# Optimization experiments

Hardware: AMD Instinct MI355X
Metric: run time of the kernel (lower is better)

## Reference

```python
import jax, jax.numpy as jnp
import numpy as np

B, C, H, W = 4, 256, 64, 64
INTER = C // 2
BN_EPS = 1e-5


def setup_inputs() -> dict:
    key = jax.random.key(0)
    ks = jax.random.split(key, 12)
    s = 0.05
    return {
        "x": jax.random.normal(ks[0], (B, C, H, W), dtype=jnp.float32),
        "theta_w": jax.random.normal(ks[1], (INTER, C), dtype=jnp.float32) * s,
        "theta_b": jax.random.normal(ks[2], (INTER,), dtype=jnp.float32) * s,
        "phi_w": jax.random.normal(ks[3], (INTER, C), dtype=jnp.float32) * s,
        "phi_b": jax.random.normal(ks[4], (INTER,), dtype=jnp.float32) * s,
        "g_w": jax.random.normal(ks[5], (INTER, C), dtype=jnp.float32) * s,
        "g_b": jax.random.normal(ks[6], (INTER,), dtype=jnp.float32) * s,
        "W_w": jax.random.normal(ks[7], (C, INTER), dtype=jnp.float32) * s,
        "W_b": jax.random.normal(ks[8], (C,), dtype=jnp.float32) * s,
        "bn_gamma": jnp.ones((C,), dtype=jnp.float32),
        "bn_beta": jnp.zeros((C,), dtype=jnp.float32),
    }


def _conv1x1(x, w, b):
    # 1x1 conv == per-pixel GEMM: (B,C,H,W) x (O,C) -> (B,O,H,W)
    return jnp.einsum("bchw,oc->bohw", x, w) + b[None, :, None, None]


def reference(x, theta_w, theta_b, phi_w, phi_b, g_w, g_b, W_w, W_b, bn_gamma, bn_beta):
    b, c, h, w = x.shape
    hw = h * w
    theta = _conv1x1(x, theta_w, theta_b).reshape(b, -1, hw)  # (B, inter, HW) -> queries
    phi = _conv1x1(x, phi_w, phi_b).reshape(b, -1, hw)        # (B, inter, HW) -> keys
    g = _conv1x1(x, g_w, g_b).reshape(b, -1, hw)              # (B, inter, HW) -> values
    # f[n,m] = <theta[:,n], phi[:,m]> over all HW spatial positions
    f = jnp.einsum("bin,bim->bnm", theta, phi)                # (B, HW, HW)
    attn = jax.nn.softmax(f, axis=-1)
    y = jnp.einsum("bnm,bim->bin", attn, g)                   # (B, inter, HW)
    y = y.reshape(b, c // 2, h, w)
    wy = _conv1x1(y, W_w, W_b)                                # (B, C, H, W)
    # BatchNorm2d (training-mode batch statistics, per channel)
    mean = jnp.mean(wy, axis=(0, 2, 3), keepdims=True)
    var = jnp.var(wy, axis=(0, 2, 3), keepdims=True)
    wy_bn = bn_gamma[None, :, None, None] * (wy - mean) * jax.lax.rsqrt(var + BN_EPS) + bn_beta[None, :, None, None]
    return wy_bn + x
```

## Files before the change

### kernel.cpp

```cpp
#include <hip/hip_runtime.h>
#include <hip/hip_bf16.h>

#define HWN   4096
#define CIN   256
#define NINTER 128
#define NBATCH 4
#define BN_EPS 1e-5f
#define NC    4
#define CHUNK 1024
#define LOG2E 1.4426950408889634f
#define SMAX  64.0f

typedef __bf16 bf16_t;
typedef __bf16 bf16x8 __attribute__((ext_vector_type(8)));
typedef __bf16 bf16x4 __attribute__((ext_vector_type(4)));
typedef float  f32x4  __attribute__((ext_vector_type(4)));
typedef float  f32x16 __attribute__((ext_vector_type(16)));

__device__ __forceinline__ float fexp2(float x) {
  return __builtin_amdgcn_exp2f(x);
}

__device__ __forceinline__ void split_bf16(float v, bf16_t& h, bf16_t& l) {
  h = (bf16_t)v;
  l = (bf16_t)(v - (float)h);
}

#define OFF_QH  0
#define OFF_KH  4194304
#define OFF_V   8388608
#define OFF_OP  12582912
#define OFF_WY  46137344
#define OFF_LP  54525952
#define OFF_WBF 54790144
#define OFF_ST  55314432

__global__ __launch_bounds__(256) void convert_weights(
    const float* __restrict__ tw, const float* __restrict__ pw,
    const float* __restrict__ gw, const float* __restrict__ ww,
    bf16_t* __restrict__ out) {
  int i = blockIdx.x * 256 + threadIdx.x;
  float v;
  if (i < 32768)        v = tw[i];
  else if (i < 65536)   v = pw[i - 32768];
  else if (i < 98304)   v = gw[i - 65536];
  else                  v = ww[i - 98304];
  bf16_t h, l;
  split_bf16(v, h, l);
  out[i] = h;
  out[131072 + i] = l;
}

__global__ __launch_bounds__(256, 4) void qkv_kernel(
    const float* __restrict__ x, const bf16_t* __restrict__ wbf,
    const float* __restrict__ tb, const float* __restrict__ pb,
    const float* __restrict__ gb,
    bf16_t* __restrict__ Qh, bf16_t* __restrict__ Kh, bf16_t* __restrict__ V) {
  const int ntb  = blockIdx.x;
  const int b    = blockIdx.y;
  const int tid  = threadIdx.x;
  const int lane = tid & 63;
  const int wv   = tid >> 6;
  const int l31  = lane & 31;
  const int half = lane >> 5;

  __shared__ __align__(16) bf16_t smem[4608];
  bf16_t (*xTh)[72] = (bf16_t(*)[72])smem;
  bf16_t (*xTl)[72] = (bf16_t(*)[72])(smem + 2304);
  bf16_t (*Tr)[136] = (bf16_t(*)[136])smem;

  const bf16_t* Th = wbf;
  const bf16_t* Tl = wbf + 131072;
  const bf16_t* Ph = wbf + 32768;
  const bf16_t* Pl = wbf + 131072 + 32768;
  const bf16_t* Gh = wbf + 65536;
  const float*  xb = x + (size_t)b * CIN * HWN + ntb * 32;

  f32x16 aq, ak, av;
#pragma unroll
  for (int i = 0; i < 16; i++) { aq[i] = 0.f; ak[i] = 0.f; av[i] = 0.f; }

  for (int c0 = 0; c0 < 256; c0 += 64) {
    __syncthreads();
#pragma unroll
    for (int i = 0; i < 8; i++) {
      int idx = tid + i * 256;
      int cc = idx >> 5;
      int nn = idx & 31;
      float v = xb[(size_t)(c0 + cc) * HWN + nn];
      bf16_t h, l;
      split_bf16(v, h, l);
      xTh[nn][cc] = h;
      xTl[nn][cc] = l;
    }
    __syncthreads();
#pragma unroll
    for (int kk = 0; kk < 64; kk += 16) {
      size_t woff = (size_t)(32 * wv + l31) * 256 + c0 + kk + half * 8;
      bf16x8 th = *(const bf16x8*)(Th + woff);
      bf16x8 tl = *(const bf16x8*)(Tl + woff);
      bf16x8 ph = *(const bf16x8*)(Ph + woff);
      bf16x8 pl = *(const bf16x8*)(Pl + woff);
      bf16x8 gh = *(const bf16x8*)(Gh + woff);
      bf16x8 bh = *(const bf16x8*)(&xTh[l31][kk + half * 8]);
      bf16x8 bl = *(const bf16x8*)(&xTl[l31][kk + half * 8]);
      aq = __builtin_amdgcn_mfma_f32_32x32x16_bf16(th, bh, aq, 0, 0, 0);
      aq = __builtin_amdgcn_mfma_f32_32x32x16_bf16(th, bl, aq, 0, 0, 0);
      aq = __builtin_amdgcn_mfma_f32_32x32x16_bf16(tl, bh, aq, 0, 0, 0);
      ak = __builtin_amdgcn_mfma_f32_32x32x16_bf16(ph, bh, ak, 0, 0, 0);
      ak = __builtin_amdgcn_mfma_f32_32x32x16_bf16(ph, bl, ak, 0, 0, 0);
      ak = __builtin_amdgcn_mfma_f32_32x32x16_bf16(pl, bh, ak, 0, 0, 0);
      av = __builtin_amdgcn_mfma_f32_32x32x16_bf16(gh, bh, av, 0, 0, 0);
    }
  }

  const int trow = tid >> 3;
  const int tc16 = (tid & 7) * 16;
  bf16_t* qh = Qh + ((size_t)b * HWN + ntb * 32) * NINTER;
  bf16_t* kh = Kh + ((size_t)b * HWN + ntb * 32) * NINTER;

#pragma unroll
  for (int rnd = 0; rnd < 2; rnd++) {
    __syncthreads();
#pragma unroll
    for (int rg = 0; rg < 4; rg++) {
      int och0 = 32 * wv + 8 * rg + 4 * half;
#pragma unroll
      for (int j = 0; j < 4; j++) {
        float v = (rnd == 0) ? (aq[rg * 4 + j] + tb[och0 + j]) * LOG2E
                             : (ak[rg * 4 + j] + pb[och0 + j]);
        Tr[l31][och0 + j] = (bf16_t)v;
      }
    }
    __syncthreads();
    bf16_t* dst = (rnd == 0) ? qh : kh;
    bf16x8 v0 = *(const bf16x8*)(&Tr[trow][tc16]);
    bf16x8 v1 = *(const bf16x8*)(&Tr[trow][tc16 + 8]);
    *(bf16x8*)(dst + (size_t)trow * NINTER + tc16) = v0;
    *(bf16x8*)(dst + (size_t)trow * NINTER + tc16 + 8) = v1;
  }

  const int n = ntb * 32 + l31;
  bf16_t* vd = V + (size_t)b * NINTER * HWN;
#pragma unroll
  for (int r = 0; r < 16; r++) {
    int och = 32 * wv + (r & 3) + 8 * (r >> 2) + 4 * half;
    vd[(size_t)och * HWN + n] = (bf16_t)(av[r] + gb[och]);
  }
}

__global__ __launch_bounds__(256, 2) void attn_kernel(
    const bf16_t* __restrict__ Qh, const bf16_t* __restrict__ Kh,
    const bf16_t* __restrict__ V,
    float* __restrict__ Opart, float* __restrict__ Lp) {
  const int qt    = blockIdx.x;
  const int chunk = blockIdx.y;
  const int b     = blockIdx.z;
  const int tid   = threadIdx.x;
  const int lane  = tid & 63;
  const int wv    = tid >> 6;
  const int l15   = lane & 15;
  const int quad  = lane >> 4;
  const int kbase = chunk * CHUNK;

  __shared__ __align__(16) bf16_t Klds[32][136];
  __shared__ __align__(16) bf16_t Vlds[144][56];
  __shared__ __align__(16) bf16_t Plds[4][32][40];

  const bf16_t* Qhb = Qh + (size_t)b * HWN * NINTER;
  const bf16_t* Khb = Kh + (size_t)b * HWN * NINTER;
  const bf16_t* Vb  = V + (size_t)b * NINTER * HWN;

  if (tid < 112) {
    int row = 128 + tid / 7;
    int c8 = (tid % 7) * 8;
    bf16x8 v;
#pragma unroll
    for (int j = 0; j < 8; j++) v[j] = (bf16_t)((row == 128) ? 1.0f : 0.0f);
    *(bf16x8*)(&Vlds[row][c8]) = v;
  }

  bf16x8 qf[2][4];
#pragma unroll
  for (int qs = 0; qs < 2; qs++) {
    const int qrow = qt * 128 + wv * 32 + qs * 16 + l15;
#pragma unroll
    for (int kc = 0; kc < 4; kc++)
      qf[qs][kc] = *(const bf16x8*)(Qhb + (size_t)qrow * NINTER + kc * 32 + quad * 8);
  }

  f32x4 o[2][8], ol[2];
#pragma unroll
  for (int qs = 0; qs < 2; qs++) {
#pragma unroll
    for (int dt = 0; dt < 8; dt++)
#pragma unroll
      for (int i = 0; i < 4; i++) o[qs][dt][i] = 0.f;
#pragma unroll
    for (int i = 0; i < 4; i++) ol[qs][i] = 0.f;
  }

  for (int t = 0; t < 32; t++) {
    __syncthreads();
#pragma unroll
    for (int i = 0; i < 2; i++) {
      int idx = tid + i * 256;
      int row = idx >> 4;
      int c8 = (idx & 15) * 8;
      *(uint4*)(&Klds[row][c8]) =
          *(const uint4*)(Khb + (size_t)(kbase + t * 32 + row) * NINTER + c8);
    }
#pragma unroll
    for (int i = 0; i < 2; i++) {
      int idx = tid + i * 256;
      int row = idx >> 2;
      int c8 = (idx & 3) * 8;
      *(uint4*)(&Vlds[row][c8]) =
          *(const uint4*)(Vb + (size_t)row * HWN + kbase + t * 32 + c8);
    }
    __syncthreads();

    f32x4 s[2][2];
#pragma unroll
    for (int qs = 0; qs < 2; qs++)
#pragma unroll
      for (int ks = 0; ks < 2; ks++)
#pragma unroll
        for (int i = 0; i < 4; i++) s[qs][ks][i] = 0.f;
#pragma unroll
    for (int ks = 0; ks < 2; ks++)
#pragma unroll
      for (int kc = 0; kc < 4; kc++) {
        bf16x8 kf = *(const bf16x8*)(&Klds[ks * 16 + l15][kc * 32 + quad * 8]);
        s[0][ks] = __builtin_amdgcn_mfma_f32_16x16x32_bf16(kf, qf[0][kc], s[0][ks], 0, 0, 0);
        s[1][ks] = __builtin_amdgcn_mfma_f32_16x16x32_bf16(kf, qf[1][kc], s[1][ks], 0, 0, 0);
      }

#pragma unroll
    for (int qs = 0; qs < 2; qs++)
#pragma unroll
      for (int ks = 0; ks < 2; ks++) {
        bf16x4 p4;
#pragma unroll
        for (int r = 0; r < 4; r++)
          p4[r] = (bf16_t)fexp2(s[qs][ks][r] - SMAX);
        *(bf16x4*)(&Plds[wv][qs * 16 + l15][ks * 16 + quad * 4]) = p4;
      }

    bf16x8 pf0 = *(const bf16x8*)(&Plds[wv][l15][quad * 8]);
    bf16x8 pf1 = *(const bf16x8*)(&Plds[wv][16 + l15][quad * 8]);
#pragma unroll
    for (int dt = 0; dt < 8; dt++) {
      bf16x8 vf = *(const bf16x8*)(&Vlds[dt * 16 + l15][quad * 8]);
      o[0][dt] = __builtin_amdgcn_mfma_f32_16x16x32_bf16(pf0, vf, o[0][dt], 0, 0, 0);
      o[1][dt] = __builtin_amdgcn_mfma_f32_16x16x32_bf16(pf1, vf, o[1][dt], 0, 0, 0);
    }
    bf16x8 vfl = *(const bf16x8*)(&Vlds[128 + l15][quad * 8]);
    ol[0] = __builtin_amdgcn_mfma_f32_16x16x32_bf16(pf0, vfl, ol[0], 0, 0, 0);
    ol[1] = __builtin_amdgcn_mfma_f32_16x16x32_bf16(pf1, vfl, ol[1], 0, 0, 0);
  }

  float* Ob = Opart + ((size_t)(b * NC + chunk) * HWN) * NINTER;
#pragma unroll
  for (int qs = 0; qs < 2; qs++)
#pragma unroll
    for (int r = 0; r < 4; r++) {
      int n = qt * 128 + wv * 32 + qs * 16 + quad * 4 + r;
#pragma unroll
      for (int dt = 0; dt < 8; dt++)
        Ob[(size_t)n * NINTER + dt * 16 + l15] = o[qs][dt][r];
      if (l15 == 0)
        Lp[(size_t)(b * NC + chunk) * HWN + n] = ol[qs][r];
    }
}

__global__ __launch_bounds__(256, 4) void wconv_kernel(
    const bf16_t* __restrict__ Wbf, const float* __restrict__ Opart,
    const float* __restrict__ Lp, const float* __restrict__ Wb,
    bf16_t* __restrict__ WY) {
  const int ntb = blockIdx.x;
  const int b   = blockIdx.y;
  const int tid = threadIdx.x;
  const int lane = tid & 63;
  const int wv   = tid >> 6;
  const int l31  = lane & 31;
  const int half = lane >> 5;

  __shared__ __align__(16) bf16_t Ylds[32][136];
  __shared__ float Linv[32];

  if (tid < 32) {
    int n = ntb * 32 + tid;
    float ls = 0.f;
#pragma unroll
    for (int c = 0; c < NC; c++) ls += Lp[(size_t)(b * NC + c) * HWN + n];
    Linv[tid] = 1.f / ls;
  }

  const int nrow = tid >> 3;
  const int dgrp = tid & 7;
  float oacc[16];
#pragma unroll
  for (int j = 0; j < 16; j++) oacc[j] = 0.f;
#pragma unroll
  for (int c = 0; c < NC; c++) {
    const float* Op = Opart +
        ((size_t)(b * NC + c) * HWN + ntb * 32 + nrow) * NINTER + dgrp * 16;
#pragma unroll
    for (int q = 0; q < 4; q++) {
      f32x4 v = *(const f32x4*)(Op + q * 4);
#pragma unroll
      for (int j = 0; j < 4; j++) oacc[q * 4 + j] += v[j];
    }
  }
  __syncthreads();
  {
    float inv = Linv[nrow];
    bf16x8 y0, y1;
#pragma unroll
    for (int j = 0; j < 8; j++) {
      y0[j] = (bf16_t)(oacc[j] * inv);
      y1[j] = (bf16_t)(oacc[8 + j] * inv);
    }
    *(bf16x8*)(&Ylds[nrow][dgrp * 16]) = y0;
    *(bf16x8*)(&Ylds[nrow][dgrp * 16 + 8]) = y1;
  }
  __syncthreads();

  const bf16_t* Wh = Wbf + 98304;
  f32x16 acc[2];
#pragma unroll
  for (int c = 0; c < 2; c++)
#pragma unroll
    for (int i = 0; i < 16; i++) acc[c][i] = 0.f;

#pragma unroll
  for (int k0 = 0; k0 < 128; k0 += 16) {
    bf16x8 a0 = *(const bf16x8*)(Wh + (size_t)(wv * 64 + l31) * NINTER + k0 + half * 8);
    bf16x8 a1 = *(const bf16x8*)(Wh + (size_t)(wv * 64 + 32 + l31) * NINTER + k0 + half * 8);
    bf16x8 b0 = *(const bf16x8*)(&Ylds[l31][k0 + half * 8]);
    acc[0] = __builtin_amdgcn_mfma_f32_32x32x16_bf16(a0, b0, acc[0], 0, 0, 0);
    acc[1] = __builtin_amdgcn_mfma_f32_32x32x16_bf16(a1, b0, acc[1], 0, 0, 0);
  }

  bf16_t* dst = WY + (size_t)b * 256 * HWN + ntb * 32;
#pragma unroll
  for (int ct = 0; ct < 2; ct++)
#pragma unroll
    for (int r = 0; r < 16; r++) {
      int co = wv * 64 + ct * 32 + (r & 3) + 8 * (r >> 2) + 4 * half;
      dst[(size_t)co * HWN + l31] = (bf16_t)(acc[ct][r] + Wb[co]);
    }
}

__global__ __launch_bounds__(256) void stats_kernel(
    const bf16_t* __restrict__ WY, float* __restrict__ stats) {
  const int c = blockIdx.x;
  const int tid = threadIdx.x;
  float s = 0.f, s2 = 0.f;
  for (int b = 0; b < NBATCH; b++) {
    const bf16_t* p = WY + ((size_t)b * 256 + c) * HWN;
    for (int i = tid * 8; i < HWN; i += 2048) {
      bf16x8 v8 = *(const bf16x8*)(p + i);
#pragma unroll
      for (int j = 0; j < 8; j++) {
        float v = (float)v8[j];
        s += v;
        s2 += v * v;
      }
    }
  }
#pragma unroll
  for (int off = 1; off < 64; off <<= 1) {
    s += __shfl_xor(s, off);
    s2 += __shfl_xor(s2, off);
  }
  __shared__ float red[8];
  int wv = tid >> 6;
  if ((tid & 63) == 0) { red[wv] = s; red[4 + wv] = s2; }
  __syncthreads();
  if (tid == 0) {
    float S = red[0] + red[1] + red[2] + red[3];
    float S2 = red[4] + red[5] + red[6] + red[7];
    float mean = S * (1.f / 16384.f);
    float var = S2 * (1.f / 16384.f) - mean * mean;
    stats[c] = mean;
    stats[256 + c] = rsqrtf(var + BN_EPS);
  }
}

__global__ __launch_bounds__(256) void bn_kernel(
    const bf16_t* __restrict__ WY, const float* __restrict__ x,
    const float* __restrict__ stats, const float* __restrict__ gamma,
    const float* __restrict__ beta, float* __restrict__ out) {
  int idx = blockIdx.x * 256 + threadIdx.x;
  int e = idx * 4;
  int c = (e >> 12) & 255;
  bf16x4 w4 = *(const bf16x4*)(WY + e);
  float4 xv = *(const float4*)(x + e);
  float mean = stats[c];
  float g = gamma[c] * stats[256 + c];
  float bb = beta[c];
  float4 o;
  o.x = g * ((float)w4[0] - mean) + bb + xv.x;
  o.y = g * ((float)w4[1] - mean) + bb + xv.y;
  o.z = g * ((float)w4[2] - mean) + bb + xv.z;
  o.w = g * ((float)w4[3] - mean) + bb + xv.w;
  *(float4*)(out + e) = o;
}

extern "C" void kernel_launch(void* const* d_in, const int* in_sizes, int n_in,
                              void* d_out, int out_size, void* d_ws, size_t ws_size,
                              hipStream_t stream) {
  const float* x       = (const float*)d_in[0];
  const float* theta_b = (const float*)d_in[2];
  const float* phi_b   = (const float*)d_in[4];
  const float* g_b     = (const float*)d_in[6];
  const float* W_b     = (const float*)d_in[8];
  const float* bn_g    = (const float*)d_in[9];
  const float* bn_b    = (const float*)d_in[10];
  float* out = (float*)d_out;

  char* ws = (char*)d_ws;
  bf16_t* Qh  = (bf16_t*)(ws + OFF_QH);
  bf16_t* Kh  = (bf16_t*)(ws + OFF_KH);
  bf16_t* V   = (bf16_t*)(ws + OFF_V);
  float*  OP  = (float*)(ws + OFF_OP);
  bf16_t* WY  = (bf16_t*)(ws + OFF_WY);
  float*  LP  = (float*)(ws + OFF_LP);
  bf16_t* WBF = (bf16_t*)(ws + OFF_WBF);
  float*  ST  = (float*)(ws + OFF_ST);

  convert_weights<<<512, 256, 0, stream>>>(
      (const float*)d_in[1], (const float*)d_in[3],
      (const float*)d_in[5], (const float*)d_in[7], WBF);
  qkv_kernel<<<dim3(128, NBATCH), 256, 0, stream>>>(
      x, WBF, theta_b, phi_b, g_b, Qh, Kh, V);
  attn_kernel<<<dim3(32, NC, NBATCH), 256, 0, stream>>>(
      Qh, Kh, V, OP, LP);
  wconv_kernel<<<dim3(128, NBATCH), 256, 0, stream>>>(
      WBF, OP, LP, W_b, WY);
  stats_kernel<<<256, 256, 0, stream>>>(WY, ST);
  bn_kernel<<<4096, 256, 0, stream>>>(WY, x, ST, bn_g, bn_b, out);
}
```

Baseline: 180.8 us.

## Register-prefetch K/V tiles in attention and split keys into eight chunks

The attention loop now prefetches the next K/V tile into registers while the current tile is computed from LDS, ping-ponging between two register sets with explicit barriers and scheduling fences. The key split becomes a template parameter, and eight chunks are used when the workspace is large enough, which doubles the grid to give more parallelism. Launch bounds rise to three blocks per SM. The aim is to hide global load latency and raise occupancy, at the cost of more register pressure and twice the partial-output traffic and reduction work in wconv.

```diff
diff --git a/kernel.cpp b/kernel.cpp
--- a/kernel.cpp
+++ b/kernel.cpp
@@ -6,8 +6,6 @@
 #define NINTER 128
 #define NBATCH 4
 #define BN_EPS 1e-5f
-#define NC    4
-#define CHUNK 1024
 #define LOG2E 1.4426950408889634f
 #define SMAX  64.0f
 
@@ -25,15 +23,6 @@
   h = (bf16_t)v;
   l = (bf16_t)(v - (float)h);
 }
-
-#define OFF_QH  0
-#define OFF_KH  4194304
-#define OFF_V   8388608
-#define OFF_OP  12582912
-#define OFF_WY  46137344
-#define OFF_LP  54525952
-#define OFF_WBF 54790144
-#define OFF_ST  55314432
 
 __global__ __launch_bounds__(256) void convert_weights(
     const float* __restrict__ tw, const float* __restrict__ pw,
@@ -149,10 +138,13 @@
   }
 }
 
-__global__ __launch_bounds__(256, 2) void attn_kernel(
+template<int NCv>
+__global__ __launch_bounds__(256, 3) void attn_kernel(
     const bf16_t* __restrict__ Qh, const bf16_t* __restrict__ Kh,
     const bf16_t* __restrict__ V,
     float* __restrict__ Opart, float* __restrict__ Lp) {
+  constexpr int CH = HWN / NCv;
+  constexpr int NT = CH / 32;
   const int qt    = blockIdx.x;
   const int chunk = blockIdx.y;
   const int b     = blockIdx.z;
@@ -161,7 +153,7 @@
   const int wv    = tid >> 6;
   const int l15   = lane & 15;
   const int quad  = lane >> 4;
-  const int kbase = chunk * CHUNK;
+  const int kbase = chunk * CH;
 
   __shared__ __align__(16) bf16_t Klds[32][136];
   __shared__ __align__(16) bf16_t Vlds[144][56];
@@ -200,26 +192,32 @@
     for (int i = 0; i < 4; i++) ol[qs][i] = 0.f;
   }
 
-  for (int t = 0; t < 32; t++) {
-    __syncthreads();
+  auto load_tile = [&](uint4* kr, uint4* vr, int t) {
 #pragma unroll
     for (int i = 0; i < 2; i++) {
       int idx = tid + i * 256;
-      int row = idx >> 4;
-      int c8 = (idx & 15) * 8;
-      *(uint4*)(&Klds[row][c8]) =
-          *(const uint4*)(Khb + (size_t)(kbase + t * 32 + row) * NINTER + c8);
+      kr[i] = *(const uint4*)(Khb + (size_t)(kbase + t * 32 + (idx >> 4)) * NINTER + (idx & 15) * 8);
     }
 #pragma unroll
     for (int i = 0; i < 2; i++) {
       int idx = tid + i * 256;
-      int row = idx >> 2;
-      int c8 = (idx & 3) * 8;
-      *(uint4*)(&Vlds[row][c8]) =
-          *(const uint4*)(Vb + (size_t)row * HWN + kbase + t * 32 + c8);
-    }
-    __syncthreads();
-
+      vr[i] = *(const uint4*)(Vb + (size_t)(idx >> 2) * HWN + kbase + t * 32 + (idx & 3) * 8);
+    }
+  };
+  auto store_tile = [&](const uint4* kr, const uint4* vr) {
+#pragma unroll
+    for (int i = 0; i < 2; i++) {
+      int idx = tid + i * 256;
+      *(uint4*)(&Klds[idx >> 4][(idx & 15) * 8]) = kr[i];
+    }
+#pragma unroll
+    for (int i = 0; i < 2; i++) {
+      int idx = tid + i * 256;
+      *(uint4*)(&Vlds[idx >> 2][(idx & 3) * 8]) = vr[i];
+    }
+  };
+
+  auto compute = [&]() {
     f32x4 s[2][2];
 #pragma unroll
     for (int qs = 0; qs < 2; qs++)
@@ -258,9 +256,39 @@
     bf16x8 vfl = *(const bf16x8*)(&Vlds[128 + l15][quad * 8]);
     ol[0] = __builtin_amdgcn_mfma_f32_16x16x32_bf16(pf0, vfl, ol[0], 0, 0, 0);
     ol[1] = __builtin_amdgcn_mfma_f32_16x16x32_bf16(pf1, vfl, ol[1], 0, 0, 0);
-  }
-
-  float* Ob = Opart + ((size_t)(b * NC + chunk) * HWN) * NINTER;
+  };
+
+  uint4 krA[2], vrA[2], krB[2], vrB[2];
+  load_tile(krA, vrA, 0);
+
+#pragma unroll 1
+  for (int t = 0; t < NT; t += 2) {
+    __builtin_amdgcn_s_barrier();
+    __builtin_amdgcn_sched_barrier(0);
+    store_tile(krA, vrA);
+    __builtin_amdgcn_sched_barrier(0);
+    load_tile(krB, vrB, t + 1);
+    __builtin_amdgcn_sched_barrier(0);
+    asm volatile("s_waitcnt lgkmcnt(0)" ::: "memory");
+    __builtin_amdgcn_sched_barrier(0);
+    __builtin_amdgcn_s_barrier();
+    __builtin_amdgcn_sched_barrier(0);
+    compute();
+
+    __builtin_amdgcn_s_barrier();
+    __builtin_amdgcn_sched_barrier(0);
+    store_tile(krB, vrB);
+    __builtin_amdgcn_sched_barrier(0);
+    if (t + 2 < NT) load_tile(krA, vrA, t + 2);
+    __builtin_amdgcn_sched_barrier(0);
+    asm volatile("s_waitcnt lgkmcnt(0)" ::: "memory");
+    __builtin_amdgcn_sched_barrier(0);
+    __builtin_amdgcn_s_barrier();
+    __builtin_amdgcn_sched_barrier(0);
+    compute();
+  }
+
+  float* Ob = Opart + ((size_t)(b * NCv + chunk) * HWN) * NINTER;
 #pragma unroll
   for (int qs = 0; qs < 2; qs++)
 #pragma unroll
@@ -270,10 +298,11 @@
       for (int dt = 0; dt < 8; dt++)
         Ob[(size_t)n * NINTER + dt * 16 + l15] = o[qs][dt][r];
       if (l15 == 0)
-        Lp[(size_t)(b * NC + chunk) * HWN + n] = ol[qs][r];
-    }
-}
-
+        Lp[(size_t)(b * NCv + chunk) * HWN + n] = ol[qs][r];
+    }
+}
+
+template<int NCv>
 __global__ __launch_bounds__(256, 4) void wconv_kernel(
     const bf16_t* __restrict__ Wbf, const float* __restrict__ Opart,
     const float* __restrict__ Lp, const float* __restrict__ Wb,
@@ -293,7 +322,7 @@
     int n = ntb * 32 + tid;
     float ls = 0.f;
 #pragma unroll
-    for (int c = 0; c < NC; c++) ls += Lp[(size_t)(b * NC + c) * HWN + n];
+    for (int c = 0; c < NCv; c++) ls += Lp[(size_t)(b * NCv + c) * HWN + n];
     Linv[tid] = 1.f / ls;
   }
 
@@ -303,9 +332,9 @@
 #pragma unroll
   for (int j = 0; j < 16; j++) oacc[j] = 0.f;
 #pragma unroll
-  for (int c = 0; c < NC; c++) {
+  for (int c = 0; c < NCv; c++) {
     const float* Op = Opart +
-        ((size_t)(b * NC + c) * HWN + ntb * 32 + nrow) * NINTER + dgrp * 16;
+        ((size_t)(b * NCv + c) * HWN + ntb * 32 + nrow) * NINTER + dgrp * 16;
 #pragma unroll
     for (int q = 0; q < 4; q++) {
       f32x4 v = *(const f32x4*)(Op + q * 4);
@@ -421,25 +450,34 @@
   const float* bn_b    = (const float*)d_in[10];
   float* out = (float*)d_out;
 
+  const size_t NEED8 = 12582912ull + 67108864ull + 8388608ull + 524288ull +
+                       524288ull + 2048ull;
+  const int nc = (ws_size >= NEED8) ? 8 : 4;
+  const size_t opb = (size_t)nc * HWN * NINTER * NBATCH * 4;
+  const size_t lpb = (size_t)nc * HWN * NBATCH * 4;
+
   char* ws = (char*)d_ws;
-  bf16_t* Qh  = (bf16_t*)(ws + OFF_QH);
-  bf16_t* Kh  = (bf16_t*)(ws + OFF_KH);
-  bf16_t* V   = (bf16_t*)(ws + OFF_V);
-  float*  OP  = (float*)(ws + OFF_OP);
-  bf16_t* WY  = (bf16_t*)(ws + OFF_WY);
-  float*  LP  = (float*)(ws + OFF_LP);
-  bf16_t* WBF = (bf16_t*)(ws + OFF_WBF);
-  float*  ST  = (float*)(ws + OFF_ST);
+  bf16_t* Qh  = (bf16_t*)(ws);
+  bf16_t* Kh  = (bf16_t*)(ws + 4194304);
+  bf16_t* V   = (bf16_t*)(ws + 8388608);
+  float*  OP  = (float*)(ws + 12582912);
+  bf16_t* WY  = (bf16_t*)(ws + 12582912 + opb);
+  float*  LP  = (float*)(ws + 12582912 + opb + 8388608);
+  bf16_t* WBF = (bf16_t*)(ws + 12582912 + opb + 8388608 + lpb);
+  float*  ST  = (float*)(ws + 12582912 + opb + 8388608 + lpb + 524288);
 
   convert_weights<<<512, 256, 0, stream>>>(
       (const float*)d_in[1], (const float*)d_in[3],
       (const float*)d_in[5], (const float*)d_in[7], WBF);
   qkv_kernel<<<dim3(128, NBATCH), 256, 0, stream>>>(
       x, WBF, theta_b, phi_b, g_b, Qh, Kh, V);
-  attn_kernel<<<dim3(32, NC, NBATCH), 256, 0, stream>>>(
-      Qh, Kh, V, OP, LP);
-  wconv_kernel<<<dim3(128, NBATCH), 256, 0, stream>>>(
-      WBF, OP, LP, W_b, WY);
+  if (nc == 8) {
+    attn_kernel<8><<<dim3(32, 8, NBATCH), 256, 0, stream>>>(Qh, Kh, V, OP, LP);
+    wconv_kernel<8><<<dim3(128, NBATCH), 256, 0, stream>>>(WBF, OP, LP, W_b, WY);
+  } else {
+    attn_kernel<4><<<dim3(32, 4, NBATCH), 256, 0, stream>>>(Qh, Kh, V, OP, LP);
+    wconv_kernel<4><<<dim3(128, NBATCH), 256, 0, stream>>>(WBF, OP, LP, W_b, WY);
+  }
   stats_kernel<<<256, 256, 0, stream>>>(WY, ST);
   bn_kernel<<<4096, 256, 0, stream>>>(WY, x, ST, bn_g, bn_b, out);
 }
```

After: 209.8 us. 1.16x slower.
